# Optimization experiments

Hardware: AMD Instinct MI355X
Metric: run time of the kernel (lower is better)

The kernel has to match this reference:

```python
import jax, jax.numpy as jnp
import numpy as np

B, NS, NT, C = 32, 1000, 100, 256
LAMBDA_GIOU, LAMBDA_L1 = 10.0, 1.0


def _lsa(cost):
    """Hungarian / Jonker-Volgenant shortest-augmenting-path (numpy, O(n^2 m)).
    Matches scipy.optimize.linear_sum_assignment for rectangular matrices."""
    cost = np.asarray(cost, dtype=np.float64)
    transposed = cost.shape[0] > cost.shape[1]
    if transposed:
        cost = cost.T
    n, m = cost.shape  # n <= m
    INF = np.inf
    u = np.zeros(n + 1)
    v = np.zeros(m + 1)
    p = np.zeros(m + 1, dtype=np.int64)   # p[j] = row (1-based) assigned to col j
    way = np.zeros(m + 1, dtype=np.int64)
    for i in range(1, n + 1):
        p[0] = i
        j0 = 0
        minv = np.full(m + 1, INF)
        used = np.zeros(m + 1, dtype=bool)
        while True:
            used[j0] = True
            i0 = p[j0]
            cur = cost[i0 - 1, :] - u[i0] - v[1:]
            free = ~used[1:]
            better = free & (cur < minv[1:])
            minv[1:][better] = cur[better]
            way[1:][better] = j0
            masked = np.where(free, minv[1:], INF)
            j1 = int(np.argmin(masked)) + 1
            delta = masked[j1 - 1]
            u[p[used]] += delta
            v[used] -= delta
            minv[~used] -= delta
            j0 = j1
            if p[j0] == 0:
                break
        while j0:
            j1 = way[j0]
            p[j0] = p[j1]
            j0 = j1
    rows = p[1:] - 1
    cols = np.arange(m)
    keep = rows >= 0
    rows, cols = rows[keep], cols[keep]
    if transposed:
        rows, cols = cols, rows
    order = np.argsort(rows)
    return rows[order], cols[order]


def _pairwise_cost(logits, classes, sb, tb):
    """Per-batch (Ns,Nt) cost = CE(logits_s, class_t) + 10*(1-GIoU(box_s, box_t)) + L1mean."""
    Bc, Ns, Cd = logits.shape
    Nt = classes.shape[1]
    # Cross entropy: logsumexp over classes minus logit at target class (identical
    # math to the torch expand+flatten CE, without the Ns*Nt*C copy).
    lse = jax.nn.logsumexp(logits, axis=-1)  # (B,Ns)
    picked = jnp.take_along_axis(
        logits, jnp.broadcast_to(classes[:, None, :], (Bc, Ns, Nt)), axis=2)  # (B,Ns,Nt)
    ce = lse[:, :, None] - picked
    # Pairwise GIoU (boxes in xyxy)
    s = sb[:, :, None, :]  # (B,Ns,1,4)
    t = tb[:, None, :, :]  # (B,1,Nt,4)
    ix1 = jnp.maximum(s[..., 0], t[..., 0])
    iy1 = jnp.maximum(s[..., 1], t[..., 1])
    ix2 = jnp.minimum(s[..., 2], t[..., 2])
    iy2 = jnp.minimum(s[..., 3], t[..., 3])
    inter = jnp.clip(ix2 - ix1, 0.0) * jnp.clip(iy2 - iy1, 0.0)
    area_s = (s[..., 2] - s[..., 0]) * (s[..., 3] - s[..., 1])
    area_t = (t[..., 2] - t[..., 0]) * (t[..., 3] - t[..., 1])
    union = area_s + area_t - inter
    iou = inter / union
    cx1 = jnp.minimum(s[..., 0], t[..., 0])
    cy1 = jnp.minimum(s[..., 1], t[..., 1])
    cx2 = jnp.maximum(s[..., 2], t[..., 2])
    cy2 = jnp.maximum(s[..., 3], t[..., 3])
    carea = (cx2 - cx1) * (cy2 - cy1)
    giou = iou - (carea - union) / carea
    l1 = jnp.abs(s - t).mean(axis=-1)  # (B,Ns,Nt)
    return ce + LAMBDA_GIOU * (1.0 - giou) + LAMBDA_L1 * l1


def _valid_boxes(key, b, n):
    p = jax.random.uniform(key, (b, n, 2, 2), dtype=jnp.float32)
    lo = p.min(axis=2)
    hi = p.max(axis=2)
    return jnp.concatenate([lo, hi], axis=-1)  # (b,n,4) xyxy, x1<x2, y1<y2


def setup_inputs() -> dict:
    key = jax.random.key(0)
    k1, k2, k3, k4 = jax.random.split(key, 4)
    return {
        "source_class_logits": jax.random.normal(k1, (B, NS, C), dtype=jnp.float32),
        "target_classes": jax.random.randint(k2, (B, NT), 0, C, dtype=jnp.int32),
        "source_boxes": _valid_boxes(k3, B, NS),
        "target_boxes": _valid_boxes(k4, B, NT),
    }


def reference(source_class_logits, target_classes, source_boxes, target_boxes):
    cost = _pairwise_cost(source_class_logits, target_classes, source_boxes, target_boxes)
    cost_np = np.asarray(cost)
    rows_l, cols_l = [], []
    for b in range(cost_np.shape[0]):  # assignment is inherently per-matrix / host-side
        r, c = _lsa(cost_np[b])
        rows_l.append(r)
        cols_l.append(c)
    rows = jnp.asarray(np.stack(rows_l))  # (B, min(Ns,Nt))
    cols = jnp.asarray(np.stack(cols_l))
    bidx = jnp.arange(cost.shape[0])[:, None]
    return cost[bidx, rows, cols].mean(axis=1)  # (B,)
```

## Files before the change

### kernel.cpp

```cpp
#include <hip/hip_runtime.h>
#include <math.h>

#define NSRC 1000
#define NTGT 100
#define NCLS 256
#define NB   32
#define NSP  1024
#define PAD_IDX(j) ((j) + ((j) >> 4))
#define LDSN (NSP + (NSP >> 4))
#define AUCTION_EPS 0.04f
#define NWAVES 8
#define ROUND_CAP 96


__global__ __launch_bounds__(256) void lse_kernel(const float* __restrict__ logits,
                                                  float* __restrict__ lse) {
    int wid  = threadIdx.x >> 6;
    int lane = threadIdx.x & 63;
    int row0 = blockIdx.x * 32 + wid * 8;
    #pragma unroll 2
    for (int r = 0; r < 8; ++r) {
        int row = row0 + r;
        float4 v4 = reinterpret_cast<const float4*>(logits + (size_t)row * NCLS)[lane];
        float m = fmaxf(fmaxf(v4.x, v4.y), fmaxf(v4.z, v4.w));
        #pragma unroll
        for (int off = 32; off >= 1; off >>= 1) m = fmaxf(m, __shfl_xor(m, off));
        float s = expf(v4.x - m) + expf(v4.y - m) + expf(v4.z - m) + expf(v4.w - m);
        #pragma unroll
        for (int off = 32; off >= 1; off >>= 1) s += __shfl_xor(s, off);
        if (lane == 0) lse[row] = m + logf(s);
    }
}

__global__ __launch_bounds__(256) void cost_kernel(const float* __restrict__ logits,
                                                   const int*   __restrict__ tcls,
                                                   const float* __restrict__ sbox,
                                                   const float* __restrict__ tbox,
                                                   const float* __restrict__ lse,
                                                   float*       __restrict__ cost,
                                                   float*       __restrict__ urow_g,
                                                   int*         __restrict__ jmin_g,
                                                   float*       __restrict__ m2_g) {
    int b  = blockIdx.x & 31;
    int t  = blockIdx.x >> 5;
    int bt = b * NTGT + t;
    int cls = tcls[bt];
    float4 tb = reinterpret_cast<const float4*>(tbox)[bt];
    float area_t = (tb.z - tb.x) * (tb.w - tb.y);
    float* crow = cost + (size_t)bt * NSP;
    float m1 = 1e38f, m2 = 1e38f; int mi = 0x7fffffff;
    for (int s = threadIdx.x; s < NSP; s += 256) {
        if (s >= NSRC) { crow[s] = 1e30f; continue; }
        int gs = b * NSRC + s;
        float4 sb = reinterpret_cast<const float4*>(sbox)[gs];
        float ce = lse[gs] - logits[(size_t)gs * NCLS + cls];
        float ix1 = fmaxf(sb.x, tb.x), iy1 = fmaxf(sb.y, tb.y);
        float ix2 = fminf(sb.z, tb.z), iy2 = fminf(sb.w, tb.w);
        float inter = fmaxf(ix2 - ix1, 0.f) * fmaxf(iy2 - iy1, 0.f);
        float area_s = (sb.z - sb.x) * (sb.w - sb.y);
        float uni = area_s + area_t - inter;
        float iou = inter / uni;
        float cx1 = fminf(sb.x, tb.x), cy1 = fminf(sb.y, tb.y);
        float cx2 = fmaxf(sb.z, tb.z), cy2 = fmaxf(sb.w, tb.w);
        float carea = (cx2 - cx1) * (cy2 - cy1);
        float giou = iou - (carea - uni) / carea;
        float l1 = 0.25f * (fabsf(sb.x - tb.x) + fabsf(sb.y - tb.y) +
                            fabsf(sb.z - tb.z) + fabsf(sb.w - tb.w));
        float c = ce + 10.0f * (1.0f - giou) + l1;
        crow[s] = c;
        if (c < m1) { m2 = m1; m1 = c; mi = s; }
        else if (c < m2) m2 = c;
    }
    #pragma unroll
    for (int off = 32; off >= 1; off >>= 1) {
        float om1 = __shfl_xor(m1, off);
        float om2 = __shfl_xor(m2, off);
        int   oi  = __shfl_xor(mi, off);
        bool take = (om1 < m1) || (om1 == m1 && oi < mi);
        float lose = take ? m1 : om1;
        m1 = take ? om1 : m1;
        mi = take ? oi  : mi;
        m2 = fminf(fminf(m2, om2), lose);
    }
    __shared__ float smin[4], smin2[4];
    __shared__ int   sidx[4];
    int wid = threadIdx.x >> 6, lane = threadIdx.x & 63;
    if (lane == 0) { smin[wid] = m1; smin2[wid] = m2; sidx[wid] = mi; }
    __syncthreads();
    if (threadIdx.x == 0) {
        #pragma unroll
        for (int w = 1; w < 4; ++w) {
            float om1 = smin[w], om2 = smin2[w]; int oi = sidx[w];
            bool take = (om1 < m1) || (om1 == m1 && oi < mi);
            float lose = take ? m1 : om1;
            m1 = take ? om1 : m1;
            mi = take ? oi  : mi;
            m2 = fminf(fminf(m2, om2), lose);
        }
        urow_g[bt] = m1;
        jmin_g[bt] = mi;
        m2_g[bt]   = m2;
    }
}

__global__ __launch_bounds__(512) void lsa_kernel(const float* __restrict__ cost,
                                                  const float* __restrict__ urow_g,
                                                  const int*   __restrict__ jmin_g,
                                                  const float* __restrict__ m2_g,
                                                  float* __restrict__ out) {
    int b    = blockIdx.x;
    int tid  = threadIdx.x;
    int wv   = tid >> 6;
    int lane = tid & 63;
    const float* C = cost + (size_t)b * NTGT * NSP;
    __shared__ int   way[LDSN];
    __shared__ int   pcol[LDSN];
    __shared__ float uu[LDSN];
    __shared__ float vsh[LDSN];
    __shared__ float urow[NTGT];
    __shared__ int   done[NTGT];
    __shared__ float bm1[NTGT];
    __shared__ float bm2[NTGT];
    __shared__ int   bj [NTGT];
    __shared__ float bv [NTGT];
    __shared__ int   qbuf[1024];
    __shared__ int   qstate[2];
    __shared__ int   srow[NWAVES];

    for (int t = tid; t < LDSN; t += 512) {
        pcol[t] = -1; uu[t] = 0.f; vsh[t] = 0.f; way[t] = 0x7fffffff;
    }
    for (int t = tid; t < NTGT; t += 512) {
        float m1 = urow_g[b * NTGT + t];
        urow[t] = m1;
        bm1[t]  = m1;
        bm2[t]  = m2_g[b * NTGT + t];
        bj[t]   = jmin_g[b * NTGT + t];
        bv[t]   = 0.f;
    }
    if (tid == 0) { qstate[0] = 0; qstate[1] = 0; }
    __syncthreads();

    for (int r = tid; r < NTGT; r += 512) atomicMin(&way[PAD_IDX(bj[r])], r);
    __syncthreads();
    for (int r = tid; r < NTGT; r += 512) {
        int j = bj[r];
        int w = (way[PAD_IDX(j)] == r) ? 1 : 0;
        done[r] = w;
        if (w) { pcol[PAD_IDX(j)] = r; uu[PAD_IDX(j)] = urow[r]; }
    }
    __syncthreads();

    if (tid < 64) {
        int qt = 0;
        #pragma unroll
        for (int r0 = 0; r0 < 128; r0 += 64) {
            int r = r0 + lane;
            bool act = (r < NTGT) && !done[r];
            unsigned long long mask = __ballot(act);
            if (act) qbuf[qt + __popcll(mask & ((1ull << lane) - 1ull))] = r;
            qt += __popcll(mask);
        }
        if (lane == 0) qstate[1] = qt;
    }
    __syncthreads();

    int base = lane * 16;

    for (int round = 0; round < ROUND_CAP; ++round) {
        int qh = qstate[0], qt = qstate[1];
        int navail = qt - qh;
        if (navail <= 0) break;
        int take = navail < NWAVES ? navail : NWAVES;
        if (wv < take) {
            int i = qbuf[(qh + wv) & 1023];
            if (lane == 0) srow[wv] = i;
            float m1p = bm1[i] + (bv[i] - vsh[PAD_IDX(bj[i])]);
            if (m1p > bm2[i]) {
                const float4* row4 = reinterpret_cast<const float4*>(C + (size_t)i * NSP + base);
                float m1 = 1e38f, m2 = 1e38f; int j1 = 0x7fffffff;
                #pragma unroll
                for (int q = 0; q < 4; ++q) {
                    float4 c4 = row4[q];
                    float vals[4];
                    vals[0] = c4.x - vsh[PAD_IDX(base + 4*q + 0)];
                    vals[1] = c4.y - vsh[PAD_IDX(base + 4*q + 1)];
                    vals[2] = c4.z - vsh[PAD_IDX(base + 4*q + 2)];
                    vals[3] = c4.w - vsh[PAD_IDX(base + 4*q + 3)];
                    #pragma unroll
                    for (int e = 0; e < 4; ++e) {
                        float val = vals[e];
                        if (val < m1) { m2 = m1; m1 = val; j1 = base + 4*q + e; }
                        else m2 = fminf(m2, val);
                    }
                }
                #pragma unroll
                for (int off = 32; off >= 1; off >>= 1) {
                    float om1 = __shfl_xor(m1, off);
                    float om2 = __shfl_xor(m2, off);
                    int   oj1 = __shfl_xor(j1, off);
                    bool tk = (om1 < m1) || (om1 == m1 && oj1 < j1);
                    float lose = tk ? m1 : om1;
                    m1 = tk ? om1 : m1;
                    j1 = tk ? oj1 : j1;
                    m2 = fminf(fminf(m2, om2), lose);
                }
                if (lane == 0) {
                    bm1[i] = m1; bm2[i] = m2; bj[i] = j1;
                    bv[i]  = vsh[PAD_IDX(j1)];
                }
            }
        }
        __syncthreads();
        if (tid == 0) {
            int qt2 = qstate[1];
            for (int s = 0; s < take; ++s) {
                int i  = srow[s];
                int j1 = bj[i];
                int pj1 = PAD_IDX(j1);
                float vnow = vsh[pj1];
                float m1p  = bm1[i] + (bv[i] - vnow);
                if (m1p <= bm2[i]) {
                    float delta = fmaxf(bm2[i] - m1p, AUCTION_EPS);
                    int old = pcol[pj1];
                    vsh[pj1]  = vnow - delta;
                    pcol[pj1] = i;
                    uu[pj1]   = m1p + delta;
                    urow[i]   = m1p + delta;
                    done[i]   = 1;
                    if (old >= 0) { qbuf[qt2 & 1023] = old; ++qt2; done[old] = 0; }
                } else {
                    qbuf[qt2 & 1023] = i; ++qt2;
                }
            }
            qstate[0] = qstate[0] + take;
            qstate[1] = qt2;
        }
        __syncthreads();
    }

    float v[16], d[16];
    if (tid < 64) {
        #pragma unroll
        for (int k = 0; k < 16; ++k) v[k] = vsh[PAD_IDX(base + k)];
    }
    __syncthreads();

    for (int i = 0; i < NTGT; ++i) {
        if (done[i]) continue;
        float ui = urow[i];
        float Df = 0.f;
        int jf = -1;
        if (tid < 64) {
            const float4* row4 = reinterpret_cast<const float4*>(C + (size_t)i * NSP + base);
            #pragma unroll
            for (int q = 0; q < 4; ++q) {
                float4 c4 = row4[q];
                d[4*q+0] = c4.x - ui - v[4*q+0];
                d[4*q+1] = c4.y - ui - v[4*q+1];
                d[4*q+2] = c4.z - ui - v[4*q+2];
                d[4*q+3] = c4.w - ui - v[4*q+3];
            }
            #pragma unroll
            for (int k = 0; k < 16; ++k) way[PAD_IDX(base + k)] = -1;
            unsigned int used = 0;
            int   pf_j = -1;
            float pfr[16];

            for (int it = 0; it < NTGT + 3; ++it) {
                float l1 = 1e38f, l2 = 1e38f;
                int   i1 = 0x7fffffff, i2 = 0x7fffffff;
                #pragma unroll
                for (int k = 0; k < 16; ++k) {
                    float val = ((used >> k) & 1u) ? 1e38f : d[k];
                    int idx = base + k;
                    if (val < l1) { l2 = l1; i2 = i1; l1 = val; i1 = idx; }
                    else if (val < l2) { l2 = val; i2 = idx; }
                }
                #pragma unroll
                for (int off = 32; off >= 1; off >>= 1) {
                    float ob1 = __shfl_xor(l1, off), ob2 = __shfl_xor(l2, off);
                    int   oc1 = __shfl_xor(i1, off), oc2 = __shfl_xor(i2, off);
                    bool tk = (ob1 < l1) || (ob1 == l1 && oc1 < i1);
                    float n1 = tk ? ob1 : l1; int ni1 = tk ? oc1 : i1;
                    float lz = tk ? l1  : ob1; int liz = tk ? i1  : oc1;
                    float n2 = lz; int ni2 = liz;
                    if (l2  < n2) { n2 = l2;  ni2 = i2;  }
                    if (ob2 < n2) { n2 = ob2; ni2 = oc2; }
                    l1 = n1; i1 = ni1; l2 = n2; i2 = ni2;
                }
                float wmin = l1; int j0 = i1; int j0b = i2;
                if (wmin >= 1e37f) break;
                int pj0 = pcol[PAD_IDX(j0)];
                if (pj0 < 0) { Df = wmin; jf = j0; break; }
                if ((j0 >> 4) == lane) used |= 1u << (j0 & 15);
                float uref = uu[PAD_IDX(j0)];
                float sft  = wmin - uref;
                float cr[16];
                if (pf_j == j0) {
                    #pragma unroll
                    for (int k = 0; k < 16; ++k) cr[k] = pfr[k];
                    pf_j = -1;
                } else {
                    const float4* rr = reinterpret_cast<const float4*>(C + (size_t)pj0 * NSP + base);
                    #pragma unroll
                    for (int q = 0; q < 4; ++q) {
                        float4 c4 = rr[q];
                        cr[4*q+0] = c4.x; cr[4*q+1] = c4.y; cr[4*q+2] = c4.z; cr[4*q+3] = c4.w;
                    }
                }
                if (j0b < NSP && j0b != pf_j) {
                    int pj0b = pcol[PAD_IDX(j0b)];
                    if (pj0b >= 0) {
                        const float4* rb = reinterpret_cast<const float4*>(C + (size_t)pj0b * NSP + base);
                        #pragma unroll
                        for (int q = 0; q < 4; ++q) {
                            float4 c4 = rb[q];
                            pfr[4*q+0] = c4.x; pfr[4*q+1] = c4.y;
                            pfr[4*q+2] = c4.z; pfr[4*q+3] = c4.w;
                        }
                        pf_j = j0b;
                    } else pf_j = -1;
                }
                #pragma unroll
                for (int k = 0; k < 16; ++k) {
                    float cand = sft + cr[k] - v[k];
                    bool upd = (cand < d[k]) && !((used >> k) & 1u);
                    if (upd) { d[k] = cand; way[PAD_IDX(base + k)] = j0; }
                }
            }

            if (jf >= 0) {
                #pragma unroll
                for (int k = 0; k < 16; ++k) {
                    if ((used >> k) & 1u) {
                        float diff = Df - d[k];
                        v[k] -= diff;
                        uu[PAD_IDX(base + k)] += diff;
                    }
                }
            }
        }
        __syncthreads();
        if (tid == 0 && jf >= 0) {
            int j = jf;
            for (int g = 0; g < NSP; ++g) {
                int jp = way[PAD_IDX(j)];
                if (jp < 0) { pcol[PAD_IDX(j)] = i; uu[PAD_IDX(j)] = ui + Df; break; }
                pcol[PAD_IDX(j)] = pcol[PAD_IDX(jp)];
                uu[PAD_IDX(j)]   = uu[PAD_IDX(jp)];
                j = jp;
            }
            done[i] = 1;
        }
        __syncthreads();
    }

    if (tid < 64) {
        float acc = 0.f;
        #pragma unroll
        for (int k = 0; k < 16; ++k) {
            int j = base + k;
            if (j < NSRC) {
                int r = pcol[PAD_IDX(j)];
                if (r >= 0) acc += C[(size_t)r * NSP + j];
            }
        }
        #pragma unroll
        for (int off = 32; off >= 1; off >>= 1) acc += __shfl_xor(acc, off);
        if (lane == 0) out[b] = acc * (1.0f / NTGT);
    }
}

extern "C" void kernel_launch(void* const* d_in, const int* in_sizes, int n_in,
                              void* d_out, int out_size, void* d_ws, size_t ws_size,
                              hipStream_t stream) {
    const float* logits = (const float*)d_in[0];
    const int*   tcls   = (const int*)  d_in[1];
    const float* sbox   = (const float*)d_in[2];
    const float* tbox   = (const float*)d_in[3];
    float* out = (float*)d_out;

    float* lse    = (float*)d_ws;
    float* cost   = lse + 32768;
    float* urow_g = cost + (size_t)NB * NTGT * NSP;
    int*   jmin_g = (int*)(urow_g + NB * NTGT);
    float* m2_g   = (float*)(jmin_g + NB * NTGT);

    lse_kernel <<<1000,      256, 0, stream>>>(logits, lse);
    cost_kernel<<<NB * NTGT, 256, 0, stream>>>(logits, tcls, sbox, tbox, lse, cost,
                                               urow_g, jmin_g, m2_g);
    lsa_kernel <<<NB,        512, 0, stream>>>(cost, urow_g, jmin_g, m2_g, out);
}
```

Before: 126.8 us.

## Run auction phase in a single wave with LDS-prefetched evicted rows

The LSA kernel now runs as one 64-lane wavefront. The parallel 8-wave auction rounds, with their block barriers and serial thread-0 commit, are replaced by a sequential Gauss-Seidel auction loop that needs no __syncthreads. When a row is outbid and requeued, its cost row is prefetched asynchronously into a 16-slot LDS cache through global_load_lds, so its later rescan reads LDS instead of global memory. This trades wave-level parallelism across rows for much lower sync overhead and latency hiding. The larger LDS footprint (64KB cache) and step cap may change convergence behavior.

Measured after the change: 137.1 us. +8.2%, slower.

```diff
diff --git a/kernel.cpp b/kernel.cpp
--- a/kernel.cpp
+++ b/kernel.cpp
@@ -9,8 +9,8 @@
 #define PAD_IDX(j) ((j) + ((j) >> 4))
 #define LDSN (NSP + (NSP >> 4))
 #define AUCTION_EPS 0.04f
-#define NWAVES 8
-#define ROUND_CAP 96
+#define STEP_CAP 1500
+#define NSLOT 16
 
 
 __global__ __launch_bounds__(256) void lse_kernel(const float* __restrict__ logits,
@@ -103,16 +103,27 @@
     }
 }
 
-__global__ __launch_bounds__(512) void lsa_kernel(const float* __restrict__ cost,
-                                                  const float* __restrict__ urow_g,
-                                                  const int*   __restrict__ jmin_g,
-                                                  const float* __restrict__ m2_g,
-                                                  float* __restrict__ out) {
+__device__ __forceinline__ void stage16(const float* g, float* l) {
+#if __has_builtin(__builtin_amdgcn_global_load_lds)
+    __builtin_amdgcn_global_load_lds(
+        (const __attribute__((address_space(1))) void*)g,
+        (__attribute__((address_space(3))) void*)l, 16, 0, 0);
+#else
+    int lane = threadIdx.x & 63;
+    reinterpret_cast<float4*>(l)[lane] =
+        reinterpret_cast<const float4*>(g)[lane];
+#endif
+}
+
+__global__ __launch_bounds__(64) void lsa_kernel(const float* __restrict__ cost,
+                                                 const float* __restrict__ urow_g,
+                                                 const int*   __restrict__ jmin_g,
+                                                 const float* __restrict__ m2_g,
+                                                 float* __restrict__ out) {
     int b    = blockIdx.x;
-    int tid  = threadIdx.x;
-    int wv   = tid >> 6;
-    int lane = tid & 63;
+    int lane = threadIdx.x;
     const float* C = cost + (size_t)b * NTGT * NSP;
+    __shared__ float rowcache[NSLOT][NSP];
     __shared__ int   way[LDSN];
     __shared__ int   pcol[LDSN];
     __shared__ float uu[LDSN];
@@ -123,27 +134,28 @@
     __shared__ float bm2[NTGT];
     __shared__ int   bj [NTGT];
     __shared__ float bv [NTGT];
+    __shared__ int   cslot[NTGT];
+    __shared__ int   cown[NSLOT];
     __shared__ int   qbuf[1024];
-    __shared__ int   qstate[2];
-    __shared__ int   srow[NWAVES];
-
-    for (int t = tid; t < LDSN; t += 512) {
+
+    for (int t = lane; t < LDSN; t += 64) {
         pcol[t] = -1; uu[t] = 0.f; vsh[t] = 0.f; way[t] = 0x7fffffff;
     }
-    for (int t = tid; t < NTGT; t += 512) {
+    for (int t = lane; t < NTGT; t += 64) {
         float m1 = urow_g[b * NTGT + t];
         urow[t] = m1;
         bm1[t]  = m1;
         bm2[t]  = m2_g[b * NTGT + t];
         bj[t]   = jmin_g[b * NTGT + t];
         bv[t]   = 0.f;
-    }
-    if (tid == 0) { qstate[0] = 0; qstate[1] = 0; }
-    __syncthreads();
-
-    for (int r = tid; r < NTGT; r += 512) atomicMin(&way[PAD_IDX(bj[r])], r);
-    __syncthreads();
-    for (int r = tid; r < NTGT; r += 512) {
+        cslot[t] = -1;
+    }
+    if (lane < NSLOT) cown[lane] = -1;
+    __syncthreads();
+
+    for (int r = lane; r < NTGT; r += 64) atomicMin(&way[PAD_IDX(bj[r])], r);
+    __syncthreads();
+    for (int r = lane; r < NTGT; r += 64) {
         int j = bj[r];
         int w = (way[PAD_IDX(j)] == r) ? 1 : 0;
         done[r] = w;
@@ -151,34 +163,44 @@
     }
     __syncthreads();
 
-    if (tid < 64) {
-        int qt = 0;
-        #pragma unroll
-        for (int r0 = 0; r0 < 128; r0 += 64) {
-            int r = r0 + lane;
-            bool act = (r < NTGT) && !done[r];
-            unsigned long long mask = __ballot(act);
-            if (act) qbuf[qt + __popcll(mask & ((1ull << lane) - 1ull))] = r;
-            qt += __popcll(mask);
-        }
-        if (lane == 0) qstate[1] = qt;
+    int qt = 0;
+    #pragma unroll
+    for (int r0 = 0; r0 < 128; r0 += 64) {
+        int r = r0 + lane;
+        bool act = (r < NTGT) && !done[r];
+        unsigned long long mask = __ballot(act);
+        if (act) qbuf[qt + __popcll(mask & ((1ull << lane) - 1ull))] = r;
+        qt += __popcll(mask);
     }
     __syncthreads();
 
     int base = lane * 16;
-
-    for (int round = 0; round < ROUND_CAP; ++round) {
-        int qh = qstate[0], qt = qstate[1];
-        int navail = qt - qh;
-        if (navail <= 0) break;
-        int take = navail < NWAVES ? navail : NWAVES;
-        if (wv < take) {
-            int i = qbuf[(qh + wv) & 1023];
-            if (lane == 0) srow[wv] = i;
-            float m1p = bm1[i] + (bv[i] - vsh[PAD_IDX(bj[i])]);
-            if (m1p > bm2[i]) {
+    int qh = 0, nextslot = 0;
+
+    for (int step = 0; qh < qt && step < STEP_CAP; ++step) {
+        __threadfence_block();
+        int   i    = qbuf[qh & 1023];
+        ++qh;
+        int   j1   = bj[i];
+        float vnow = vsh[PAD_IDX(j1)];
+        float m1p  = bm1[i] + (bv[i] - vnow);
+        float m2v  = bm2[i];
+        if (m1p > m2v) {
+            float m1 = 1e38f, m2 = 1e38f; int jj = 0x7fffffff;
+            int slot = cslot[i];
+            if (slot >= 0) {
+                asm volatile("s_waitcnt vmcnt(0)" ::: "memory");
+                __threadfence_block();
+                const float* rc = rowcache[slot];
+                #pragma unroll
+                for (int e = 0; e < 16; ++e) {
+                    int j = lane + (e << 6);
+                    float val = rc[j] - vsh[PAD_IDX(j)];
+                    if (val < m1) { m2 = m1; m1 = val; jj = j; }
+                    else m2 = fminf(m2, val);
+                }
+            } else {
                 const float4* row4 = reinterpret_cast<const float4*>(C + (size_t)i * NSP + base);
-                float m1 = 1e38f, m2 = 1e38f; int j1 = 0x7fffffff;
                 #pragma unroll
                 for (int q = 0; q < 4; ++q) {
                     float4 c4 = row4[q];
@@ -190,60 +212,58 @@
                     #pragma unroll
                     for (int e = 0; e < 4; ++e) {
                         float val = vals[e];
-                        if (val < m1) { m2 = m1; m1 = val; j1 = base + 4*q + e; }
+                        int   idx = base + 4*q + e;
+                        if (val < m1) { m2 = m1; m1 = val; jj = idx; }
                         else m2 = fminf(m2, val);
                     }
                 }
-                #pragma unroll
-                for (int off = 32; off >= 1; off >>= 1) {
-                    float om1 = __shfl_xor(m1, off);
-                    float om2 = __shfl_xor(m2, off);
-                    int   oj1 = __shfl_xor(j1, off);
-                    bool tk = (om1 < m1) || (om1 == m1 && oj1 < j1);
-                    float lose = tk ? m1 : om1;
-                    m1 = tk ? om1 : m1;
-                    j1 = tk ? oj1 : j1;
-                    m2 = fminf(fminf(m2, om2), lose);
-                }
-                if (lane == 0) {
-                    bm1[i] = m1; bm2[i] = m2; bj[i] = j1;
-                    bv[i]  = vsh[PAD_IDX(j1)];
-                }
-            }
-        }
-        __syncthreads();
-        if (tid == 0) {
-            int qt2 = qstate[1];
-            for (int s = 0; s < take; ++s) {
-                int i  = srow[s];
-                int j1 = bj[i];
-                int pj1 = PAD_IDX(j1);
-                float vnow = vsh[pj1];
-                float m1p  = bm1[i] + (bv[i] - vnow);
-                if (m1p <= bm2[i]) {
-                    float delta = fmaxf(bm2[i] - m1p, AUCTION_EPS);
-                    int old = pcol[pj1];
-                    vsh[pj1]  = vnow - delta;
-                    pcol[pj1] = i;
-                    uu[pj1]   = m1p + delta;
-                    urow[i]   = m1p + delta;
-                    done[i]   = 1;
-                    if (old >= 0) { qbuf[qt2 & 1023] = old; ++qt2; done[old] = 0; }
-                } else {
-                    qbuf[qt2 & 1023] = i; ++qt2;
-                }
-            }
-            qstate[0] = qstate[0] + take;
-            qstate[1] = qt2;
-        }
-        __syncthreads();
-    }
+            }
+            #pragma unroll
+            for (int off = 32; off >= 1; off >>= 1) {
+                float om1 = __shfl_xor(m1, off);
+                float om2 = __shfl_xor(m2, off);
+                int   oj1 = __shfl_xor(jj, off);
+                bool tk = (om1 < m1) || (om1 == m1 && oj1 < jj);
+                float lose = tk ? m1 : om1;
+                m1 = tk ? om1 : m1;
+                jj = tk ? oj1 : jj;
+                m2 = fminf(fminf(m2, om2), lose);
+            }
+            j1 = jj; m1p = m1; m2v = m2;
+            vnow = vsh[PAD_IDX(j1)];
+            if (lane == 0) { bm1[i] = m1; bm2[i] = m2; bj[i] = j1; bv[i] = vnow; }
+        }
+        float delta = fmaxf(m2v - m1p, AUCTION_EPS);
+        int   pj1   = PAD_IDX(j1);
+        int   old   = pcol[pj1];
+        if (lane == 0) {
+            vsh[pj1]  = vnow - delta;
+            pcol[pj1] = i;
+            uu[pj1]   = m1p + delta;
+            urow[i]   = m1p + delta;
+            done[i]   = 1;
+        }
+        if (old >= 0) {
+            if (lane == 0) { qbuf[qt & 1023] = old; done[old] = 0; }
+            int s = nextslot & (NSLOT - 1);
+            ++nextslot;
+            if (lane == 0) {
+                int prev = cown[s];
+                if (prev >= 0 && cslot[prev] == s) cslot[prev] = -1;
+                cown[s] = old; cslot[old] = s;
+            }
+            const float* grow = C + (size_t)old * NSP;
+            #pragma unroll
+            for (int q = 0; q < 4; ++q)
+                stage16(grow + q * 256 + lane * 4, &rowcache[s][q * 256]);
+            ++qt;
+        }
+    }
+    __syncthreads();
 
     float v[16], d[16];
-    if (tid < 64) {
-        #pragma unroll
-        for (int k = 0; k < 16; ++k) v[k] = vsh[PAD_IDX(base + k)];
-    }
+    #pragma unroll
+    for (int k = 0; k < 16; ++k) v[k] = vsh[PAD_IDX(base + k)];
     __syncthreads();
 
     for (int i = 0; i < NTGT; ++i) {
@@ -251,7 +271,7 @@
         float ui = urow[i];
         float Df = 0.f;
         int jf = -1;
-        if (tid < 64) {
+        {
             const float4* row4 = reinterpret_cast<const float4*>(C + (size_t)i * NSP + base);
             #pragma unroll
             for (int q = 0; q < 4; ++q) {
@@ -342,7 +362,7 @@
             }
         }
         __syncthreads();
-        if (tid == 0 && jf >= 0) {
+        if (lane == 0 && jf >= 0) {
             int j = jf;
             for (int g = 0; g < NSP; ++g) {
                 int jp = way[PAD_IDX(j)];
@@ -356,20 +376,18 @@
         __syncthreads();
     }
 
-    if (tid < 64) {
-        float acc = 0.f;
-        #pragma unroll
-        for (int k = 0; k < 16; ++k) {
-            int j = base + k;
-            if (j < NSRC) {
-                int r = pcol[PAD_IDX(j)];
-                if (r >= 0) acc += C[(size_t)r * NSP + j];
-            }
-        }
-        #pragma unroll
-        for (int off = 32; off >= 1; off >>= 1) acc += __shfl_xor(acc, off);
-        if (lane == 0) out[b] = acc * (1.0f / NTGT);
-    }
+    float acc = 0.f;
+    #pragma unroll
+    for (int k = 0; k < 16; ++k) {
+        int j = base + k;
+        if (j < NSRC) {
+            int r = pcol[PAD_IDX(j)];
+            if (r >= 0) acc += C[(size_t)r * NSP + j];
+        }
+    }
+    #pragma unroll
+    for (int off = 32; off >= 1; off >>= 1) acc += __shfl_xor(acc, off);
+    if (lane == 0) out[b] = acc * (1.0f / NTGT);
 }
 
 extern "C" void kernel_launch(void* const* d_in, const int* in_sizes, int n_in,
@@ -390,5 +408,5 @@
     lse_kernel <<<1000,      256, 0, stream>>>(logits, lse);
     cost_kernel<<<NB * NTGT, 256, 0, stream>>>(logits, tcls, sbox, tbox, lse, cost,
                                                urow_g, jmin_g, m2_g);
-    lsa_kernel <<<NB,        512, 0, stream>>>(cost, urow_g, jmin_g, m2_g, out);
+    lsa_kernel <<<NB,        64,  0, stream>>>(cost, urow_g, jmin_g, m2_g, out);
 }
```

## Cache per-row top-8 candidates and resolve pairwise conflicts in auction

Applied to the files above, without the earlier changes.

The cost kernel now keeps each row in LDS and extracts the 8 smallest reduced costs and their columns plus a 9th-value bound. The auction bid step uses this list and falls back to a full 1024-column row scan only when the second-best value could exceed that bound. The conflict-resolution step also settles two bidders on the same column directly by comparing their gaps. This aims to cut global row reads and auction rounds, at the cost of a serial top-9 extraction per row and more LDS in the lsa kernel.

Measured after the change: 150.2 us. 1.18x slower.

```diff
diff --git a/kernel.cpp b/kernel.cpp
--- a/kernel.cpp
+++ b/kernel.cpp
@@ -38,9 +38,9 @@
                                                    const float* __restrict__ tbox,
                                                    const float* __restrict__ lse,
                                                    float*       __restrict__ cost,
-                                                   float*       __restrict__ urow_g,
-                                                   int*         __restrict__ jmin_g,
-                                                   float*       __restrict__ m2_g) {
+                                                   float*       __restrict__ topv,
+                                                   int*         __restrict__ topj) {
+    __shared__ float srow[NSP];
     int b  = blockIdx.x & 31;
     int t  = blockIdx.x >> 5;
     int bt = b * NTGT + t;
@@ -48,9 +48,8 @@
     float4 tb = reinterpret_cast<const float4*>(tbox)[bt];
     float area_t = (tb.z - tb.x) * (tb.w - tb.y);
     float* crow = cost + (size_t)bt * NSP;
-    float m1 = 1e38f, m2 = 1e38f; int mi = 0x7fffffff;
     for (int s = threadIdx.x; s < NSP; s += 256) {
-        if (s >= NSRC) { crow[s] = 1e30f; continue; }
+        if (s >= NSRC) { crow[s] = 1e30f; srow[s] = 1e30f; continue; }
         int gs = b * NSRC + s;
         float4 sb = reinterpret_cast<const float4*>(sbox)[gs];
         float ce = lse[gs] - logits[(size_t)gs * NCLS + cls];
@@ -68,45 +67,41 @@
                             fabsf(sb.z - tb.z) + fabsf(sb.w - tb.w));
         float c = ce + 10.0f * (1.0f - giou) + l1;
         crow[s] = c;
-        if (c < m1) { m2 = m1; m1 = c; mi = s; }
-        else if (c < m2) m2 = c;
-    }
-    #pragma unroll
-    for (int off = 32; off >= 1; off >>= 1) {
-        float om1 = __shfl_xor(m1, off);
-        float om2 = __shfl_xor(m2, off);
-        int   oi  = __shfl_xor(mi, off);
-        bool take = (om1 < m1) || (om1 == m1 && oi < mi);
-        float lose = take ? m1 : om1;
-        m1 = take ? om1 : m1;
-        mi = take ? oi  : mi;
-        m2 = fminf(fminf(m2, om2), lose);
-    }
-    __shared__ float smin[4], smin2[4];
-    __shared__ int   sidx[4];
-    int wid = threadIdx.x >> 6, lane = threadIdx.x & 63;
-    if (lane == 0) { smin[wid] = m1; smin2[wid] = m2; sidx[wid] = mi; }
-    __syncthreads();
-    if (threadIdx.x == 0) {
-        #pragma unroll
-        for (int w = 1; w < 4; ++w) {
-            float om1 = smin[w], om2 = smin2[w]; int oi = sidx[w];
-            bool take = (om1 < m1) || (om1 == m1 && oi < mi);
-            float lose = take ? m1 : om1;
-            m1 = take ? om1 : m1;
-            mi = take ? oi  : mi;
-            m2 = fminf(fminf(m2, om2), lose);
-        }
-        urow_g[bt] = m1;
-        jmin_g[bt] = mi;
-        m2_g[bt]   = m2;
+        srow[s] = c;
+    }
+    __syncthreads();
+    if (threadIdx.x < 64) {
+        int lane = threadIdx.x;
+        float r[16];
+        #pragma unroll
+        for (int e = 0; e < 16; ++e) r[e] = srow[lane + (e << 6)];
+        unsigned int taken = 0;
+        for (int p = 0; p < 9; ++p) {
+            float lm = 1e38f; int le = 0;
+            #pragma unroll
+            for (int e = 0; e < 16; ++e) {
+                float val = ((taken >> e) & 1u) ? 1e38f : r[e];
+                if (val < lm) { lm = val; le = e; }
+            }
+            float bmv = lm; int bi = lane + (le << 6);
+            #pragma unroll
+            for (int off = 32; off >= 1; off >>= 1) {
+                float om = __shfl_xor(bmv, off);
+                int   oi = __shfl_xor(bi, off);
+                if (om < bmv || (om == bmv && oi < bi)) { bmv = om; bi = oi; }
+            }
+            if (lane == 0) {
+                topv[bt * 9 + p] = bmv;
+                if (p < 8) topj[bt * 8 + p] = bi;
+            }
+            if ((bi & 63) == lane) taken |= 1u << (bi >> 6);
+        }
     }
 }
 
 __global__ __launch_bounds__(512) void lsa_kernel(const float* __restrict__ cost,
-                                                  const float* __restrict__ urow_g,
-                                                  const int*   __restrict__ jmin_g,
-                                                  const float* __restrict__ m2_g,
+                                                  const float* __restrict__ topv,
+                                                  const int*   __restrict__ topj,
                                                   float* __restrict__ out) {
     int b    = blockIdx.x;
     int tid  = threadIdx.x;
@@ -123,22 +118,27 @@
     __shared__ float bm2[NTGT];
     __shared__ int   bj [NTGT];
     __shared__ float bv [NTGT];
+    __shared__ float candV[NTGT * 9];
+    __shared__ int   candJ[NTGT * 8];
     __shared__ int   qbuf[1024];
     __shared__ int   qstate[2];
-    __shared__ int   srow[NWAVES];
+    __shared__ int   srow_q[NWAVES];
 
     for (int t = tid; t < LDSN; t += 512) {
         pcol[t] = -1; uu[t] = 0.f; vsh[t] = 0.f; way[t] = 0x7fffffff;
     }
+    for (int t = tid; t < NTGT * 9; t += 512) candV[t] = topv[b * NTGT * 9 + t];
+    for (int t = tid; t < NTGT * 8; t += 512) candJ[t] = topj[b * NTGT * 8 + t];
+    if (tid == 0) { qstate[0] = 0; qstate[1] = 0; }
+    __syncthreads();
     for (int t = tid; t < NTGT; t += 512) {
-        float m1 = urow_g[b * NTGT + t];
+        float m1 = candV[t * 9 + 0];
         urow[t] = m1;
         bm1[t]  = m1;
-        bm2[t]  = m2_g[b * NTGT + t];
-        bj[t]   = jmin_g[b * NTGT + t];
+        bm2[t]  = candV[t * 9 + 1];
+        bj[t]   = candJ[t * 8 + 0];
         bv[t]   = 0.f;
     }
-    if (tid == 0) { qstate[0] = 0; qstate[1] = 0; }
     __syncthreads();
 
     for (int r = tid; r < NTGT; r += 512) atomicMin(&way[PAD_IDX(bj[r])], r);
@@ -174,40 +174,56 @@
         int take = navail < NWAVES ? navail : NWAVES;
         if (wv < take) {
             int i = qbuf[(qh + wv) & 1023];
-            if (lane == 0) srow[wv] = i;
+            if (lane == 0) srow_q[wv] = i;
             float m1p = bm1[i] + (bv[i] - vsh[PAD_IDX(bj[i])]);
             if (m1p > bm2[i]) {
-                const float4* row4 = reinterpret_cast<const float4*>(C + (size_t)i * NSP + base);
                 float m1 = 1e38f, m2 = 1e38f; int j1 = 0x7fffffff;
                 #pragma unroll
-                for (int q = 0; q < 4; ++q) {
-                    float4 c4 = row4[q];
-                    float vals[4];
-                    vals[0] = c4.x - vsh[PAD_IDX(base + 4*q + 0)];
-                    vals[1] = c4.y - vsh[PAD_IDX(base + 4*q + 1)];
-                    vals[2] = c4.z - vsh[PAD_IDX(base + 4*q + 2)];
-                    vals[3] = c4.w - vsh[PAD_IDX(base + 4*q + 3)];
+                for (int k = 0; k < 8; ++k) {
+                    int jc = candJ[i * 8 + k];
+                    float val = candV[i * 9 + k] - vsh[PAD_IDX(jc)];
+                    if (val < m1) { m2 = m1; m1 = val; j1 = jc; }
+                    else m2 = fminf(m2, val);
+                }
+                if (m2 <= candV[i * 9 + 8]) {
+                    if (lane == 0) {
+                        bm1[i] = m1; bm2[i] = m2; bj[i] = j1;
+                        bv[i]  = vsh[PAD_IDX(j1)];
+                    }
+                } else {
+                    const float4* row4 = reinterpret_cast<const float4*>(C + (size_t)i * NSP + base);
+                    m1 = 1e38f; m2 = 1e38f; j1 = 0x7fffffff;
                     #pragma unroll
-                    for (int e = 0; e < 4; ++e) {
-                        float val = vals[e];
-                        if (val < m1) { m2 = m1; m1 = val; j1 = base + 4*q + e; }
-                        else m2 = fminf(m2, val);
-                    }
-                }
-                #pragma unroll
-                for (int off = 32; off >= 1; off >>= 1) {
-                    float om1 = __shfl_xor(m1, off);
-                    float om2 = __shfl_xor(m2, off);
-                    int   oj1 = __shfl_xor(j1, off);
-                    bool tk = (om1 < m1) || (om1 == m1 && oj1 < j1);
-                    float lose = tk ? m1 : om1;
-                    m1 = tk ? om1 : m1;
-                    j1 = tk ? oj1 : j1;
-                    m2 = fminf(fminf(m2, om2), lose);
-                }
-                if (lane == 0) {
-                    bm1[i] = m1; bm2[i] = m2; bj[i] = j1;
-                    bv[i]  = vsh[PAD_IDX(j1)];
+                    for (int q = 0; q < 4; ++q) {
+                        float4 c4 = row4[q];
+                        float vals[4];
+                        vals[0] = c4.x - vsh[PAD_IDX(base + 4*q + 0)];
+                        vals[1] = c4.y - vsh[PAD_IDX(base + 4*q + 1)];
+                        vals[2] = c4.z - vsh[PAD_IDX(base + 4*q + 2)];
+                        vals[3] = c4.w - vsh[PAD_IDX(base + 4*q + 3)];
+                        #pragma unroll
+                        for (int e = 0; e < 4; ++e) {
+                            float val = vals[e];
+                            int   idx = base + 4*q + e;
+                            if (val < m1) { m2 = m1; m1 = val; j1 = idx; }
+                            else m2 = fminf(m2, val);
+                        }
+                    }
+                    #pragma unroll
+                    for (int off = 32; off >= 1; off >>= 1) {
+                        float om1 = __shfl_xor(m1, off);
+                        float om2 = __shfl_xor(m2, off);
+                        int   oj1 = __shfl_xor(j1, off);
+                        bool tk = (om1 < m1) || (om1 == m1 && oj1 < j1);
+                        float lose = tk ? m1 : om1;
+                        m1 = tk ? om1 : m1;
+                        j1 = tk ? oj1 : j1;
+                        m2 = fminf(fminf(m2, om2), lose);
+                    }
+                    if (lane == 0) {
+                        bm1[i] = m1; bm2[i] = m2; bj[i] = j1;
+                        bv[i]  = vsh[PAD_IDX(j1)];
+                    }
                 }
             }
         }
@@ -215,23 +231,43 @@
         if (tid == 0) {
             int qt2 = qstate[1];
             for (int s = 0; s < take; ++s) {
-                int i  = srow[s];
+                int i  = srow_q[s];
                 int j1 = bj[i];
                 int pj1 = PAD_IDX(j1);
                 float vnow = vsh[pj1];
                 float m1p  = bm1[i] + (bv[i] - vnow);
-                if (m1p <= bm2[i]) {
-                    float delta = fmaxf(bm2[i] - m1p, AUCTION_EPS);
-                    int old = pcol[pj1];
-                    vsh[pj1]  = vnow - delta;
-                    pcol[pj1] = i;
-                    uu[pj1]   = m1p + delta;
-                    urow[i]   = m1p + delta;
-                    done[i]   = 1;
-                    if (old >= 0) { qbuf[qt2 & 1023] = old; ++qt2; done[old] = 0; }
-                } else {
-                    qbuf[qt2 & 1023] = i; ++qt2;
-                }
+                if (m1p > bm2[i]) { qbuf[qt2 & 1023] = i; ++qt2; continue; }
+                float gap_i = bm2[i] - m1p;
+                int old = pcol[pj1];
+                if (old >= 0 && bj[old] == j1) {
+                    float rc_old  = bm1[old] + (bv[old] - vnow);
+                    float gap_old = bm2[old] - rc_old;
+                    if (gap_old >= 0.f) {
+                        if (gap_i >= gap_old) {
+                            float delta = gap_old + AUCTION_EPS;
+                            vsh[pj1]  = vnow - delta;
+                            pcol[pj1] = i;
+                            uu[pj1]   = m1p + delta;
+                            urow[i]   = m1p + delta;
+                            done[i]   = 1;
+                            qbuf[qt2 & 1023] = old; ++qt2; done[old] = 0;
+                        } else {
+                            float delta = gap_i + AUCTION_EPS;
+                            vsh[pj1] = vnow - delta;
+                            uu[pj1]  = rc_old + delta;
+                            urow[old] = rc_old + delta;
+                            qbuf[qt2 & 1023] = i; ++qt2;
+                        }
+                        continue;
+                    }
+                }
+                float delta = fmaxf(gap_i, AUCTION_EPS);
+                vsh[pj1]  = vnow - delta;
+                pcol[pj1] = i;
+                uu[pj1]   = m1p + delta;
+                urow[i]   = m1p + delta;
+                done[i]   = 1;
+                if (old >= 0) { qbuf[qt2 & 1023] = old; ++qt2; done[old] = 0; }
             }
             qstate[0] = qstate[0] + take;
             qstate[1] = qt2;
@@ -381,14 +417,13 @@
     const float* tbox   = (const float*)d_in[3];
     float* out = (float*)d_out;
 
-    float* lse    = (float*)d_ws;
-    float* cost   = lse + 32768;
-    float* urow_g = cost + (size_t)NB * NTGT * NSP;
-    int*   jmin_g = (int*)(urow_g + NB * NTGT);
-    float* m2_g   = (float*)(jmin_g + NB * NTGT);
+    float* lse  = (float*)d_ws;
+    float* cost = lse + 32768;
+    float* topv = cost + (size_t)NB * NTGT * NSP;
+    int*   topj = (int*)(topv + NB * NTGT * 9);
 
     lse_kernel <<<1000,      256, 0, stream>>>(logits, lse);
     cost_kernel<<<NB * NTGT, 256, 0, stream>>>(logits, tcls, sbox, tbox, lse, cost,
-                                               urow_g, jmin_g, m2_g);
-    lsa_kernel <<<NB,        512, 0, stream>>>(cost, urow_g, jmin_g, m2_g, out);
+                                               topv, topj);
+    lsa_kernel <<<NB,        512, 0, stream>>>(cost, topv, topj, out);
 }
```
